# Kernel tuning notes

Measured on AMD Instinct MI355X. Metric: run time of the kernel, lower is better.

Reference implementation:

```python
import jax, jax.numpy as jnp
import numpy as np

N = 100000       # nodes
E = 1600000      # edges (avg degree 16)
IN_DIM = 128
HIDDEN = 128


def _glorot(key, shape):
    s = 1.0 / np.sqrt(shape[0])
    return jax.random.uniform(key, shape, minval=-s, maxval=s, dtype=jnp.float32)


def setup_inputs() -> dict:
    key = jax.random.key(0)
    ks = jax.random.split(key, 8)
    x = jax.random.normal(ks[0], (N, IN_DIM), dtype=jnp.float32)
    edge_index = jax.random.randint(ks[1], (2, E), 0, N, dtype=jnp.int32)
    W0 = _glorot(ks[2], (IN_DIM, HIDDEN))
    b0 = jnp.zeros((HIDDEN,), dtype=jnp.float32)
    W1 = _glorot(ks[3], (HIDDEN, HIDDEN))
    b1 = jnp.zeros((HIDDEN,), dtype=jnp.float32)
    W2 = _glorot(ks[4], (HIDDEN, HIDDEN))
    b2 = jnp.zeros((HIDDEN,), dtype=jnp.float32)
    return {"x": x, "edge_index": edge_index,
            "W0": W0, "b0": b0, "W1": W1, "b1": b1, "W2": W2, "b2": b2}


def _gcn_conv(x, row, col, norm, W, b):
    # x' = W x, then out[i] = sum_{j in N(i) U {i}} norm_ji * x'[j], + bias
    h = x @ W                              # [N, out]
    msg = norm[:, None] * h[row]           # [E+N, out] gather + scale
    out = jax.ops.segment_sum(msg, col, num_segments=N)  # scatter-add
    return out + b


def reference(x, edge_index, W0, b0, W1, b1, W2, b2):
    # PyG GCNConv default: add self-loops, symmetric normalization D^-1/2 A D^-1/2
    self_loops = jnp.arange(N, dtype=edge_index.dtype)
    row = jnp.concatenate([edge_index[0], self_loops])  # sources
    col = jnp.concatenate([edge_index[1], self_loops])  # destinations
    deg = jax.ops.segment_sum(jnp.ones_like(col, dtype=x.dtype), col, num_segments=N)
    dinv = jax.lax.rsqrt(deg)              # deg >= 1 thanks to self-loops
    norm = dinv[row] * dinv[col]           # [E+N]

    h = _gcn_conv(x, row, col, norm, W0, b0)
    h = jax.nn.relu(h)                     # dropout: eval mode (identity)
    h = _gcn_conv(h, row, col, norm, W1, b1)
    h = jax.nn.relu(h)
    return _gcn_conv(h, row, col, norm, W2, b2)
```

## Files before the change

### kernel.cpp

```cpp
#include <hip/hip_runtime.h>

#define HID 128
#define BR  128
#define FILL_CHUNK 2048

typedef _Float16 f16;
typedef f16 f16x2 __attribute__((ext_vector_type(2)));
typedef f16 f16x4 __attribute__((ext_vector_type(4)));
typedef f16 f16x8 __attribute__((ext_vector_type(8)));
typedef float f32x4 __attribute__((ext_vector_type(4)));

static __device__ __forceinline__ float2 h2f(unsigned int u) {
    f16x2 v;
    __builtin_memcpy(&v, &u, 4);
    return make_float2((float)v[0], (float)v[1]);
}


__global__ void k_deg_count(const int* __restrict__ col, int* __restrict__ cnt, int E, int N) {
    const int xcd = blockIdx.x & 7;
    const int chunk = blockIdx.x >> 3;
    const int per = (N + 7) >> 3;
    const int lo = xcd * per;
    const int hi = min(N, lo + per);
    const int eend = min(E, (chunk + 1) * FILL_CHUNK);
    for (int e = chunk * FILL_CHUNK + threadIdx.x; e < eend; e += 256) {
        int c = col[e];
        if (c >= lo && c < hi) atomicAdd(&cnt[c], 1);
    }
}

__global__ void k_scan_block(const int* __restrict__ cnt, int* __restrict__ excl,
                             int* __restrict__ bsum, float* __restrict__ dinv, int N) {
    __shared__ int s[256];
    int i = blockIdx.x * 256 + threadIdx.x;
    int v = (i < N) ? cnt[i] : 0;
    if (i < N) dinv[i] = 1.0f / sqrtf((float)(v + 1));
    s[threadIdx.x] = v;
    __syncthreads();
    for (int off = 1; off < 256; off <<= 1) {
        int t = (threadIdx.x >= off) ? s[threadIdx.x - off] : 0;
        __syncthreads();
        s[threadIdx.x] += t;
        __syncthreads();
    }
    if (i < N) excl[i] = s[threadIdx.x] - v;
    if (threadIdx.x == 255) bsum[blockIdx.x] = s[255];
}

__global__ __launch_bounds__(1024) void k_scan_bsum(int* __restrict__ bsum, int nb) {
    __shared__ int s[1024];
    int i = threadIdx.x;
    int v = (i < nb) ? bsum[i] : 0;
    s[i] = v;
    __syncthreads();
    for (int off = 1; off < 1024; off <<= 1) {
        int t = (i >= off) ? s[i - off] : 0;
        __syncthreads();
        s[i] += t;
        __syncthreads();
    }
    if (i < nb) bsum[i] = s[i] - v;
}

__global__ void k_scan_add(int* __restrict__ row_ptr, const int* __restrict__ bsum,
                           int* __restrict__ fill, int N, int E) {
    int i = blockIdx.x * 256 + threadIdx.x;
    if (i < N) {
        int v = row_ptr[i] + bsum[blockIdx.x];
        row_ptr[i] = v;
        fill[i] = v;
    }
    if (i == 0) row_ptr[N] = E;
}

__global__ void k_fill(const int* __restrict__ row, const int* __restrict__ col,
                       int* __restrict__ fill, int* __restrict__ csr_src, int E, int N) {
    const int xcd = blockIdx.x & 7;
    const int chunk = blockIdx.x >> 3;
    const int per = (N + 7) >> 3;
    const int lo = xcd * per;
    const int hi = min(N, lo + per);
    const int eend = min(E, (chunk + 1) * FILL_CHUNK);
    for (int e = chunk * FILL_CHUNK + threadIdx.x; e < eend; e += 256) {
        int c = col[e];
        if (c >= lo && c < hi) {
            int p = atomicAdd(&fill[c], 1);
            csr_src[p] = row[e];
        }
    }
}


__global__ void k_wprep3(const float* __restrict__ W0, const float* __restrict__ W1,
                         const float* __restrict__ W2, f16* __restrict__ out) {
    const int b = blockIdx.x;
    const int which = b >> 4;
    const float* W = which == 0 ? W0 : (which == 1 ? W1 : W2);
    f16* o = out + which * 32768;
    int i = (b & 15) * 256 + threadIdx.x;
    int k = i >> 5, n0 = (i & 31) * 4;
    float4 v = reinterpret_cast<const float4*>(W)[i];
    float vv[4] = {v.x, v.y, v.z, v.w};
#pragma unroll
    for (int e = 0; e < 4; ++e) {
        int n = n0 + e;
        int idx = (k >> 3) * 1024 + n * 8 + (k & 7);
        f16 h = (f16)vv[e];
        o[idx] = h;
        o[16384 + idx] = (f16)(vv[e] - (float)h);
    }
}


template<int MODE>
__global__ __launch_bounds__(512, 4) void k_gemm(const void* __restrict__ Xv,
                                                 const f16* __restrict__ Wt,
                                                 const float* __restrict__ dinv,
                                                 f16* __restrict__ H, int N) {
    __shared__ f16 Xs[MODE == 0 ? 2 * 16384 : 16384];
    const int t = threadIdx.x;
    const int row0 = blockIdx.x * BR;

    const int w  = t >> 6;
    const int l  = t & 63;
    const int lg = l >> 4;
    const int li = l & 15;
    const int ng = w & 3;
    const int mg = w >> 2;

    f16x8 Wh[2][4], Wl[2][4];
#pragma unroll
    for (int nb = 0; nb < 2; ++nb) {
        const int ncol = (ng * 2 + nb) * 16 + li;
#pragma unroll
        for (int ks = 0; ks < 4; ++ks) {
            const int idx = (ks * 4 + lg) * 1024 + ncol * 8;
            Wh[nb][ks] = *reinterpret_cast<const f16x8*>(&Wt[idx]);
            Wl[nb][ks] = *reinterpret_cast<const f16x8*>(&Wt[16384 + idx]);
        }
    }

    if constexpr (MODE == 0) {
        const float* X = (const float*)Xv;
        for (int i = t; i < 4096; i += 512) {
            int r = i >> 5, q = i & 31;
            int gr = row0 + r;
            float4 v = make_float4(0.f, 0.f, 0.f, 0.f);
            if (gr < N) v = reinterpret_cast<const float4*>(X + (size_t)gr * HID)[q];
            f16 h0 = (f16)v.x, h1 = (f16)v.y, h2 = (f16)v.z, h3 = (f16)v.w;
            f16 l0 = (f16)(v.x - (float)h0), l1 = (f16)(v.y - (float)h1);
            f16 l2 = (f16)(v.z - (float)h2), l3 = (f16)(v.w - (float)h3);
            int base = r * 128 + (((q >> 1) ^ (r & 7)) * 8) + (q & 1) * 4;
            *reinterpret_cast<f16x4*>(&Xs[base])         = (f16x4){h0, h1, h2, h3};
            *reinterpret_cast<f16x4*>(&Xs[16384 + base]) = (f16x4){l0, l1, l2, l3};
        }
    } else {
        const f16* X = (const f16*)Xv;
        for (int i = t; i < 2048; i += 512) {
            int r = i >> 4, q = i & 15;
            int gr = row0 + r;
            f16x8 v = {};
            if (gr < N) v = *reinterpret_cast<const f16x8*>(X + (size_t)gr * HID + q * 8);
#pragma unroll
            for (int e = 0; e < 8; ++e) v[e] = v[e] > (f16)0 ? v[e] : (f16)0;
            *reinterpret_cast<f16x8*>(&Xs[r * 128 + ((q ^ (r & 7)) * 8)]) = v;
        }
    }
    __syncthreads();

    f32x4 acc[2][4];
#pragma unroll
    for (int nb = 0; nb < 2; ++nb)
#pragma unroll
        for (int mb = 0; mb < 4; ++mb) acc[nb][mb] = (f32x4){0.f, 0.f, 0.f, 0.f};

#pragma unroll
    for (int mb = 0; mb < 4; ++mb) {
        const int arow = mg * 64 + mb * 16 + li;
#pragma unroll
        for (int ks = 0; ks < 4; ++ks) {
            const int idx = arow * 128 + (((ks * 4 + lg) ^ (arow & 7)) * 8);
            f16x8 Xh = *reinterpret_cast<const f16x8*>(&Xs[idx]);
#pragma unroll
            for (int nb = 0; nb < 2; ++nb) {
                acc[nb][mb] = __builtin_amdgcn_mfma_f32_16x16x32_f16(Wh[nb][ks], Xh, acc[nb][mb], 0, 0, 0);
                acc[nb][mb] = __builtin_amdgcn_mfma_f32_16x16x32_f16(Wl[nb][ks], Xh, acc[nb][mb], 0, 0, 0);
            }
            if constexpr (MODE == 0) {
                f16x8 Xl = *reinterpret_cast<const f16x8*>(&Xs[16384 + idx]);
#pragma unroll
                for (int nb = 0; nb < 2; ++nb)
                    acc[nb][mb] = __builtin_amdgcn_mfma_f32_16x16x32_f16(Wh[nb][ks], Xl, acc[nb][mb], 0, 0, 0);
            }
        }
    }

#pragma unroll
    for (int mb = 0; mb < 4; ++mb) {
        const int m = row0 + mg * 64 + mb * 16 + li;
        if (m < N) {
            const float d = dinv[m];
#pragma unroll
            for (int nb = 0; nb < 2; ++nb) {
                f16x4 o = {(f16)(acc[nb][mb][0] * d), (f16)(acc[nb][mb][1] * d),
                           (f16)(acc[nb][mb][2] * d), (f16)(acc[nb][mb][3] * d)};
                *reinterpret_cast<f16x4*>(&H[(size_t)m * HID + (ng * 2 + nb) * 16 + lg * 4]) = o;
            }
        }
    }
}


template<bool F16OUT>
__global__ __launch_bounds__(256) void k_agg_csr(const f16* __restrict__ h,
                                                 const int* __restrict__ csr_src,
                                                 const int* __restrict__ row_ptr,
                                                 const float* __restrict__ dinv,
                                                 const float* __restrict__ bias,
                                                 void* __restrict__ outv, int N) {
    int node = (blockIdx.x * 256 + threadIdx.x) >> 6;
    if (node >= N) return;
    int lane = threadIdx.x & 63;
    const unsigned int* h32 = reinterpret_cast<const unsigned int*>(h);

    float2 self = h2f(h32[(size_t)node * 64 + lane]);
    float accx = self.x, accy = self.y;

    int j = row_ptr[node];
    const int end = row_ptr[node + 1];

    for (; j + 8 <= end; j += 8) {
        int s0 = csr_src[j];
        int s1 = csr_src[j + 1];
        int s2 = csr_src[j + 2];
        int s3 = csr_src[j + 3];
        int s4 = csr_src[j + 4];
        int s5 = csr_src[j + 5];
        int s6 = csr_src[j + 6];
        int s7 = csr_src[j + 7];
        unsigned int u0 = h32[(size_t)s0 * 64 + lane];
        unsigned int u1 = h32[(size_t)s1 * 64 + lane];
        unsigned int u2 = h32[(size_t)s2 * 64 + lane];
        unsigned int u3 = h32[(size_t)s3 * 64 + lane];
        unsigned int u4 = h32[(size_t)s4 * 64 + lane];
        unsigned int u5 = h32[(size_t)s5 * 64 + lane];
        unsigned int u6 = h32[(size_t)s6 * 64 + lane];
        unsigned int u7 = h32[(size_t)s7 * 64 + lane];
        float2 v0 = h2f(u0), v1 = h2f(u1), v2 = h2f(u2), v3 = h2f(u3);
        float2 v4 = h2f(u4), v5 = h2f(u5), v6 = h2f(u6), v7 = h2f(u7);
        accx += ((v0.x + v1.x) + (v2.x + v3.x)) + ((v4.x + v5.x) + (v6.x + v7.x));
        accy += ((v0.y + v1.y) + (v2.y + v3.y)) + ((v4.y + v5.y) + (v6.y + v7.y));
    }
    for (; j < end; ++j) {
        float2 v = h2f(h32[(size_t)csr_src[j] * 64 + lane]);
        accx += v.x;
        accy += v.y;
    }

    float di = dinv[node];
    int c = lane * 2;
    float ox = fmaf(di, accx, bias[c]);
    float oy = fmaf(di, accy, bias[c + 1]);
    if constexpr (F16OUT) {
        f16x2 o = {(f16)ox, (f16)oy};
        *reinterpret_cast<f16x2*>((f16*)outv + (size_t)node * HID + c) = o;
    } else {
        *reinterpret_cast<float2*>((float*)outv + (size_t)node * HID + c) = make_float2(ox, oy);
    }
}


extern "C" void kernel_launch(void* const* d_in, const int* in_sizes, int n_in,
                              void* d_out, int out_size, void* d_ws, size_t ws_size,
                              hipStream_t stream) {
    const float* x  = (const float*)d_in[0];
    const int*   ei = (const int*)  d_in[1];
    const float* W0 = (const float*)d_in[2];
    const float* b0 = (const float*)d_in[3];
    const float* W1 = (const float*)d_in[4];
    const float* b1 = (const float*)d_in[5];
    const float* W2 = (const float*)d_in[6];
    const float* b2 = (const float*)d_in[7];

    const int N = in_sizes[0] / HID;
    const int E = in_sizes[1] / 2;
    const int* row = ei;
    const int* col = ei + E;

    const int nb_n = (N + 255) / 256;

    f16*   h16     = (f16*)d_ws;
    float* dinv    = (float*)(h16 + (size_t)N * HID);
    int*   cnt     = (int*)(dinv + N);
    int*   row_ptr = cnt + N;
    int*   fill    = row_ptr + (N + 1);
    int*   bsum    = fill + N;
    int*   csr_src = bsum + nb_n;
    f16*   wt      = (f16*)(csr_src + E);
    f16*   wt0     = wt;
    f16*   wt1     = wt + 32768;
    f16*   wt2     = wt + 65536;
    f16*   act     = (f16*)d_out;
    float* out     = (float*)d_out;

    const int nb_gemm = (N + BR - 1) / BR;
    const int nb_agg  = (N * 64 + 255) / 256;
    const int nb_fill = ((E + FILL_CHUNK - 1) / FILL_CHUNK) * 8;

    hipMemsetAsync(cnt, 0, (size_t)N * sizeof(int), stream);
    k_wprep3<<<48, 256, 0, stream>>>(W0, W1, W2, wt);
    k_deg_count <<<nb_fill, 256, 0, stream>>>(col, cnt, E, N);
    k_scan_block<<<nb_n, 256, 0, stream>>>(cnt, row_ptr, bsum, dinv, N);
    k_scan_bsum <<<1, 1024, 0, stream>>>(bsum, nb_n);
    k_scan_add  <<<nb_n, 256, 0, stream>>>(row_ptr, bsum, fill, N, E);
    k_fill      <<<nb_fill, 256, 0, stream>>>(row, col, fill, csr_src, E, N);

    k_gemm<0>      <<<nb_gemm, 512, 0, stream>>>(x, wt0, dinv, h16, N);
    k_agg_csr<true><<<nb_agg, 256, 0, stream>>>(h16, csr_src, row_ptr, dinv, b0, act, N);
    k_gemm<1>      <<<nb_gemm, 512, 0, stream>>>(act, wt1, dinv, h16, N);
    k_agg_csr<true><<<nb_agg, 256, 0, stream>>>(h16, csr_src, row_ptr, dinv, b1, act, N);
    k_gemm<1>      <<<nb_gemm, 512, 0, stream>>>(act, wt2, dinv, h16, N);
    k_agg_csr<false><<<nb_agg, 256, 0, stream>>>(h16, csr_src, row_ptr, dinv, b2, out, N);
}
```

Measured before the change: 450.7 us.

## Fuse ReLU and LDS swizzle into aggregation, half-wave per node with wider loads

The aggregation kernel now assigns 32 lanes per node with 8-byte gathers, so each wave handles two nodes and keeps more independent row loads in flight. ReLU and the XOR swizzle the GEMM expects in shared memory move into the aggregation epilogue. The GEMM's f16 input path therefore becomes a straight vector copy into LDS, with no per-element max and no bounds check. The trade-off is that the last GEMM block now reads past row N, inside the output buffer, and relies on those garbage rows never being stored.

```diff
diff --git a/kernel.cpp b/kernel.cpp
--- a/kernel.cpp
+++ b/kernel.cpp
@@ -156,16 +156,9 @@
             *reinterpret_cast<f16x4*>(&Xs[16384 + base]) = (f16x4){l0, l1, l2, l3};
         }
     } else {
-        const f16* X = (const f16*)Xv;
-        for (int i = t; i < 2048; i += 512) {
-            int r = i >> 4, q = i & 15;
-            int gr = row0 + r;
-            f16x8 v = {};
-            if (gr < N) v = *reinterpret_cast<const f16x8*>(X + (size_t)gr * HID + q * 8);
-#pragma unroll
-            for (int e = 0; e < 8; ++e) v[e] = v[e] > (f16)0 ? v[e] : (f16)0;
-            *reinterpret_cast<f16x8*>(&Xs[r * 128 + ((q ^ (r & 7)) * 8)]) = v;
-        }
+        const f16* src = (const f16*)Xv + (size_t)row0 * HID;
+        for (int i = t; i < 2048; i += 512)
+            *reinterpret_cast<f16x8*>(&Xs[i * 8]) = *reinterpret_cast<const f16x8*>(src + (size_t)i * 8);
     }
     __syncthreads();
 
@@ -219,13 +212,14 @@
                                                  const float* __restrict__ dinv,
                                                  const float* __restrict__ bias,
                                                  void* __restrict__ outv, int N) {
-    int node = (blockIdx.x * 256 + threadIdx.x) >> 6;
+    const int node = blockIdx.x * 8 + (threadIdx.x >> 5);
     if (node >= N) return;
-    int lane = threadIdx.x & 63;
-    const unsigned int* h32 = reinterpret_cast<const unsigned int*>(h);
-
-    float2 self = h2f(h32[(size_t)node * 64 + lane]);
-    float accx = self.x, accy = self.y;
+    const int l = threadIdx.x & 31;
+    const uint2* h2 = reinterpret_cast<const uint2*>(h);
+
+    uint2 us = h2[(size_t)node * 32 + l];
+    float2 a0 = h2f(us.x), a1 = h2f(us.y);
+    float acc0 = a0.x, acc1 = a0.y, acc2 = a1.x, acc3 = a1.y;
 
     int j = row_ptr[node];
     const int end = row_ptr[node + 1];
@@ -239,34 +233,45 @@
         int s5 = csr_src[j + 5];
         int s6 = csr_src[j + 6];
         int s7 = csr_src[j + 7];
-        unsigned int u0 = h32[(size_t)s0 * 64 + lane];
-        unsigned int u1 = h32[(size_t)s1 * 64 + lane];
-        unsigned int u2 = h32[(size_t)s2 * 64 + lane];
-        unsigned int u3 = h32[(size_t)s3 * 64 + lane];
-        unsigned int u4 = h32[(size_t)s4 * 64 + lane];
-        unsigned int u5 = h32[(size_t)s5 * 64 + lane];
-        unsigned int u6 = h32[(size_t)s6 * 64 + lane];
-        unsigned int u7 = h32[(size_t)s7 * 64 + lane];
-        float2 v0 = h2f(u0), v1 = h2f(u1), v2 = h2f(u2), v3 = h2f(u3);
-        float2 v4 = h2f(u4), v5 = h2f(u5), v6 = h2f(u6), v7 = h2f(u7);
-        accx += ((v0.x + v1.x) + (v2.x + v3.x)) + ((v4.x + v5.x) + (v6.x + v7.x));
-        accy += ((v0.y + v1.y) + (v2.y + v3.y)) + ((v4.y + v5.y) + (v6.y + v7.y));
+        uint2 u0 = h2[(size_t)s0 * 32 + l];
+        uint2 u1 = h2[(size_t)s1 * 32 + l];
+        uint2 u2 = h2[(size_t)s2 * 32 + l];
+        uint2 u3 = h2[(size_t)s3 * 32 + l];
+        uint2 u4 = h2[(size_t)s4 * 32 + l];
+        uint2 u5 = h2[(size_t)s5 * 32 + l];
+        uint2 u6 = h2[(size_t)s6 * 32 + l];
+        uint2 u7 = h2[(size_t)s7 * 32 + l];
+        float2 v0 = h2f(u0.x), w0 = h2f(u0.y), v1 = h2f(u1.x), w1 = h2f(u1.y);
+        float2 v2 = h2f(u2.x), w2 = h2f(u2.y), v3 = h2f(u3.x), w3 = h2f(u3.y);
+        float2 v4 = h2f(u4.x), w4 = h2f(u4.y), v5 = h2f(u5.x), w5 = h2f(u5.y);
+        float2 v6 = h2f(u6.x), w6 = h2f(u6.y), v7 = h2f(u7.x), w7 = h2f(u7.y);
+        acc0 += ((v0.x + v1.x) + (v2.x + v3.x)) + ((v4.x + v5.x) + (v6.x + v7.x));
+        acc1 += ((v0.y + v1.y) + (v2.y + v3.y)) + ((v4.y + v5.y) + (v6.y + v7.y));
+        acc2 += ((w0.x + w1.x) + (w2.x + w3.x)) + ((w4.x + w5.x) + (w6.x + w7.x));
+        acc3 += ((w0.y + w1.y) + (w2.y + w3.y)) + ((w4.y + w5.y) + (w6.y + w7.y));
     }
     for (; j < end; ++j) {
-        float2 v = h2f(h32[(size_t)csr_src[j] * 64 + lane]);
-        accx += v.x;
-        accy += v.y;
-    }
-
-    float di = dinv[node];
-    int c = lane * 2;
-    float ox = fmaf(di, accx, bias[c]);
-    float oy = fmaf(di, accy, bias[c + 1]);
+        uint2 u = h2[(size_t)csr_src[j] * 32 + l];
+        float2 v = h2f(u.x), w = h2f(u.y);
+        acc0 += v.x; acc1 += v.y; acc2 += w.x; acc3 += w.y;
+    }
+
+    const float di = dinv[node];
+    const float4 bv = reinterpret_cast<const float4*>(bias)[l];
+    float o0 = fmaf(di, acc0, bv.x);
+    float o1 = fmaf(di, acc1, bv.y);
+    float o2 = fmaf(di, acc2, bv.z);
+    float o3 = fmaf(di, acc3, bv.w);
+
     if constexpr (F16OUT) {
-        f16x2 o = {(f16)ox, (f16)oy};
-        *reinterpret_cast<f16x2*>((f16*)outv + (size_t)node * HID + c) = o;
+        o0 = fmaxf(o0, 0.f); o1 = fmaxf(o1, 0.f);
+        o2 = fmaxf(o2, 0.f); o3 = fmaxf(o3, 0.f);
+        const int swz = (((l >> 1) ^ (node & 7)) << 1) | (l & 1);
+        f16x4 o = {(f16)o0, (f16)o1, (f16)o2, (f16)o3};
+        *reinterpret_cast<f16x4*>((f16*)outv + (size_t)node * HID + swz * 4) = o;
     } else {
-        *reinterpret_cast<float2*>((float*)outv + (size_t)node * HID + c) = make_float2(ox, oy);
+        *reinterpret_cast<float4*>((float*)outv + (size_t)node * HID + l * 4) =
+            make_float4(o0, o1, o2, o3);
     }
 }
 
@@ -305,7 +310,7 @@
     float* out     = (float*)d_out;
 
     const int nb_gemm = (N + BR - 1) / BR;
-    const int nb_agg  = (N * 64 + 255) / 256;
+    const int nb_agg  = (N + 7) / 8;
     const int nb_fill = ((E + FILL_CHUNK - 1) / FILL_CHUNK) * 8;
 
     hipMemsetAsync(cnt, 0, (size_t)N * sizeof(int), stream);
```

Result: faster. 424.2 us (-5.9%).
